# Kernel optimization log

Measured on AMD Instinct MI355X. Metric: run time of the kernel, lower is better.

The kernel has to match this reference:

```python
import jax, jax.numpy as jnp
import numpy as np

B, S, D, Q, N, H = 2, 2048, 4096, 32, 8, 128
ROPE_THETA = 10000.0


def apply_rope(x, positions, head_dim, theta):
    # x: [B, S, heads, H], positions: [B, S] int
    half = head_dim // 2
    inv_freq = 1.0 / (theta ** (jnp.arange(half, dtype=jnp.float32) * 2.0 / head_dim))
    angles = positions.astype(jnp.float32)[..., None] * inv_freq  # [B, S, half]
    cos = jnp.cos(angles)[:, :, None, :]  # [B, S, 1, half]
    sin = jnp.sin(angles)[:, :, None, :]
    x1, x2 = x[..., :half], x[..., half:]
    return jnp.concatenate([x1 * cos - x2 * sin, x2 * cos + x1 * sin], axis=-1).astype(x.dtype)


def setup_inputs() -> dict:
    key = jax.random.key(0)
    ks = jax.random.split(key, 5)
    x = jax.random.normal(ks[0], (B, S, D), dtype=jnp.float32)
    positions = jnp.broadcast_to(jnp.arange(S, dtype=jnp.int32)[None, :], (B, S))
    scale = 0.02
    Wq = jax.random.normal(ks[1], (Q, D, H), dtype=jnp.float32) * scale
    Wk = jax.random.normal(ks[2], (N, D, H), dtype=jnp.float32) * scale
    Wv = jax.random.normal(ks[3], (N, D, H), dtype=jnp.float32) * scale
    Wo = jax.random.normal(ks[4], (Q, H, D), dtype=jnp.float32) * scale
    return {"x": x, "positions": positions, "Wq": Wq, "Wk": Wk, "Wv": Wv, "Wo": Wo}


def reference(x, positions, Wq, Wk, Wv, Wo):
    # Prefill path: QKV proj + RoPE + GQA causal attention + O proj.
    head_repeats = Q // N
    q_BSQH = jnp.einsum('BSD,QDH->BSQH', x, Wq)
    q_BSQH = apply_rope(q_BSQH, positions, H, ROPE_THETA)
    k_BSNH = jnp.einsum('BSD,NDH->BSNH', x, Wk)
    k_BSNH = apply_rope(k_BSNH, positions, H, ROPE_THETA)
    v_BSNH = jnp.einsum('BSD,NDH->BSNH', x, Wv)
    # GQA head repeat
    k_BTQH = jnp.repeat(k_BSNH, head_repeats, axis=2) if head_repeats > 1 else k_BSNH
    v_BTQH = jnp.repeat(v_BSNH, head_repeats, axis=2) if head_repeats > 1 else v_BSNH
    scores_BQST = jnp.einsum('BSQH,BTQH->BQST', q_BSQH, k_BTQH) / jnp.sqrt(jnp.float32(H))
    causal = jnp.tril(jnp.ones((1, 1, S, S), dtype=jnp.bool_))
    scores_BQST = jnp.where(causal, scores_BQST, -jnp.inf)
    weights_BQST = jax.nn.softmax(scores_BQST, axis=-1)
    out_BSQH = jnp.einsum('BQST,BTQH->BSQH', weights_BQST, v_BTQH)
    o_BSD = jnp.einsum('BSQH,QHD->BSD', out_BSQH, Wo)
    return o_BSD
```

## Files before the change

### kernel.cpp

```cpp
#include <hip/hip_runtime.h>
#include <cstdint>
#include <cstddef>

#define B_  2
#define S_  2048
#define D_  4096
#define QH_ 32
#define NH_ 8
#define HD_ 128
#define MROWS (B_ * S_)
#define NQKV  (QH_ * HD_ + 2 * NH_ * HD_)
#define KOFF  (QH_ * HD_)
#define VOFF  (QH_ * HD_ + NH_ * HD_)

typedef __attribute__((ext_vector_type(8))) short bf16x8;
typedef __attribute__((ext_vector_type(4))) float f32x4;

__device__ __forceinline__ unsigned short f2bf(float f) {
    unsigned int u = __float_as_uint(f);
    return (unsigned short)((u + 0x7FFFu + ((u >> 16) & 1u)) >> 16);
}
__device__ __forceinline__ float bf2f(unsigned short h) { return __uint_as_float(((unsigned int)h) << 16); }

__device__ __forceinline__ void gl2lds16(const void* g, void* l) {
    __builtin_amdgcn_global_load_lds(
        (const __attribute__((address_space(1))) void*)g,
        (__attribute__((address_space(3))) void*)l, 16, 0, 0);
}

__global__ __launch_bounds__(256)
void convert_bf16_kernel(const float* __restrict__ in, unsigned short* __restrict__ out)
{
    const size_t i = ((size_t)blockIdx.x * 256 + threadIdx.x) * 8;
    float4 a = *(const float4*)(in + i);
    float4 b = *(const float4*)(in + i + 4);
    uint4 o;
    o.x = (unsigned int)f2bf(a.x) | ((unsigned int)f2bf(a.y) << 16);
    o.y = (unsigned int)f2bf(a.z) | ((unsigned int)f2bf(a.w) << 16);
    o.z = (unsigned int)f2bf(b.x) | ((unsigned int)f2bf(b.y) << 16);
    o.w = (unsigned int)f2bf(b.z) | ((unsigned int)f2bf(b.w) << 16);
    *(uint4*)(out + i) = o;
}

__global__ __launch_bounds__(256)
void transpose_conv_kernel(const float* __restrict__ in, unsigned short* __restrict__ out,
                           int R, int C)
{
    __shared__ unsigned short tile[64][72];
    const int t  = threadIdx.x;
    const int c0 = blockIdx.x * 64;
    const int r0 = blockIdx.y * 64;
    in  += (size_t)blockIdx.z * R * C;
    out += (size_t)blockIdx.z * R * C;
    {
        const int rr = t >> 4;
        const int cc = (t & 15) * 4;
        #pragma unroll
        for (int p = 0; p < 4; ++p) {
            float4 v = *(const float4*)(in + (size_t)(r0 + p * 16 + rr) * C + c0 + cc);
            unsigned int lo = (unsigned int)f2bf(v.x) | ((unsigned int)f2bf(v.y) << 16);
            unsigned int hi = (unsigned int)f2bf(v.z) | ((unsigned int)f2bf(v.w) << 16);
            *(uint2*)&tile[p * 16 + rr][cc] = make_uint2(lo, hi);
        }
    }
    __syncthreads();
    {
        const int j  = t >> 3;
        const int i8 = (t & 7) * 8;
        #pragma unroll
        for (int p = 0; p < 2; ++p) {
            unsigned short tmp[8];
            #pragma unroll
            for (int e = 0; e < 8; ++e) tmp[e] = tile[i8 + e][p * 32 + j];
            *(uint4*)(out + (size_t)(c0 + p * 32 + j) * R + r0 + i8) = *(uint4*)tmp;
        }
    }
}

__global__ __launch_bounds__(256)
void transpose_v_kernel(const unsigned short* __restrict__ qkv, unsigned short* __restrict__ vt)
{
    __shared__ unsigned short tile[64][76];
    const int t  = threadIdx.x;
    const int z  = blockIdx.z;
    const int b  = z >> 3, kh = z & 7;
    const int h0 = blockIdx.x * 64;
    const int s0 = blockIdx.y * 64;
    const unsigned short* in = qkv + (size_t)(b * S_) * NQKV + VOFF + kh * HD_;
    unsigned short* outb = vt + (size_t)z * HD_ * S_;
    {
        const int rr = t >> 4;
        const int cc = (t & 15) * 4;
        #pragma unroll
        for (int p = 0; p < 4; ++p) {
            uint2 v = *(const uint2*)(in + (size_t)(s0 + p * 16 + rr) * NQKV + h0 + cc);
            *(uint2*)&tile[p * 16 + rr][cc] = v;
        }
    }
    __syncthreads();
    {
        const int j  = t >> 3;
        const int i8 = (t & 7) * 8;
        #pragma unroll
        for (int p = 0; p < 2; ++p) {
            unsigned short tmp[8];
            #pragma unroll
            for (int e = 0; e < 8; ++e) tmp[e] = tile[i8 + e][p * 32 + j];
            *(uint4*)(outb + (size_t)(h0 + p * 32 + j) * S_ + s0 + i8) = *(uint4*)tmp;
        }
    }
}

template<int CF32>
__global__ __launch_bounds__(512, 2)
void gemm256_kernel(const unsigned short* __restrict__ A,
                    const unsigned short* __restrict__ Bt,
                    void* __restrict__ Cp, int Nst, int K)
{
    __shared__ alignas(16) unsigned short lds[3][2][256][32];

    const int t = threadIdx.x, l = t & 63, w = t >> 6;
    const int gx  = gridDim.x;
    const int nwg = gx * gridDim.y;
    int lin = blockIdx.y * gx + blockIdx.x;
    lin = (lin & 7) * (nwg >> 3) + (lin >> 3);
    const int bn = (lin % gx) * 256, bm = (lin / gx) * 256;
    const int wr = w >> 2, wc = w & 3;
    const int lm = l & 15, lg = l >> 4;

    f32x4 acc[8][4];
    #pragma unroll
    for (int i = 0; i < 8; ++i)
        #pragma unroll
        for (int j = 0; j < 4; ++j) acc[i][j] = (f32x4){0.f, 0.f, 0.f, 0.f};

    const int srow = w * 16 + (l >> 2);
    const int scol = (((l & 3) - ((l >> 3) & 3)) & 3) * 8;
    const unsigned short* Asrc = A  + (size_t)(bm + srow) * K + scol;
    const unsigned short* Bsrc = Bt + (size_t)(bn + srow) * K + scol;

    const int rcol = ((lg + ((lm >> 1) & 3)) & 3) * 8;

    #define STAGE_A(tt, bb) do {                                                  \
        gl2lds16(Asrc + (size_t)(tt) * 32,                  &lds[bb][0][w*16][0]); \
        gl2lds16(Asrc + (size_t)128*K + (size_t)(tt) * 32,  &lds[bb][0][128 + w*16][0]); } while (0)
    #define STAGE_B(tt, bb) do {                                                  \
        gl2lds16(Bsrc + (size_t)(tt) * 32,                  &lds[bb][1][w*16][0]); \
        gl2lds16(Bsrc + (size_t)128*K + (size_t)(tt) * 32,  &lds[bb][1][128 + w*16][0]); } while (0)

    const int nkt = K >> 5;
    STAGE_A(0, 0); STAGE_B(0, 0);
    STAGE_A(1, 1); STAGE_B(1, 1);

    for (int kt = 0; kt < nkt; ++kt) {
        if (kt + 1 < nkt) asm volatile("s_waitcnt vmcnt(4)" ::: "memory");
        else              asm volatile("s_waitcnt vmcnt(0)" ::: "memory");
        asm volatile("s_barrier" ::: "memory");

        const unsigned short (*bufA)[32] = lds[kt % 3][0];
        const unsigned short (*bufB)[32] = lds[kt % 3][1];
        const int nb = (kt + 2) % 3;
        const bool pf = (kt + 2 < nkt);

        bf16x8 bfr[4], afr[4];
        #pragma unroll
        for (int j = 0; j < 4; ++j) bfr[j] = *(const bf16x8*)&bufB[wc * 64 + j * 16 + lm][rcol];
        #pragma unroll
        for (int i = 0; i < 4; ++i) afr[i] = *(const bf16x8*)&bufA[wr * 128 + i * 16 + lm][rcol];
        if (pf) STAGE_A(kt + 2, nb);
        #pragma unroll
        for (int i = 0; i < 4; ++i)
            #pragma unroll
            for (int j = 0; j < 4; ++j)
                acc[i][j] = __builtin_amdgcn_mfma_f32_16x16x32_bf16(afr[i], bfr[j], acc[i][j], 0, 0, 0);

        #pragma unroll
        for (int i = 0; i < 4; ++i) afr[i] = *(const bf16x8*)&bufA[wr * 128 + (i + 4) * 16 + lm][rcol];
        if (pf) STAGE_B(kt + 2, nb);
        #pragma unroll
        for (int i = 0; i < 4; ++i)
            #pragma unroll
            for (int j = 0; j < 4; ++j)
                acc[i + 4][j] = __builtin_amdgcn_mfma_f32_16x16x32_bf16(afr[i], bfr[j], acc[i + 4][j], 0, 0, 0);
    }
    #undef STAGE_A
    #undef STAGE_B

    const int lr4 = lg * 4;
    #pragma unroll
    for (int i = 0; i < 8; ++i) {
        #pragma unroll
        for (int j = 0; j < 4; ++j) {
            int row = bm + wr * 128 + i * 16 + lr4;
            int col = bn + wc * 64 + j * 16 + lm;
            #pragma unroll
            for (int jj = 0; jj < 4; ++jj) {
                if constexpr (CF32)
                    ((float*)Cp)[(size_t)(row + jj) * Nst + col] = acc[i][j][jj];
                else
                    ((unsigned short*)Cp)[(size_t)(row + jj) * Nst + col] = f2bf(acc[i][j][jj]);
            }
        }
    }
}

template<int LOG2H>
__global__ __launch_bounds__(256)
void rope_kernel(unsigned short* __restrict__ data, const int* __restrict__ positions)
{
    const int gid  = blockIdx.x * 256 + threadIdx.x;
    const int j    = gid & 63;
    const int hr   = gid >> 6;
    const int head = hr & ((1 << LOG2H) - 1);
    const int bs   = hr >> LOG2H;
    const float pos = (float)positions[bs];
    const float inv = expf(-0.14391156831f * (float)j);
    float s, c;
    sincosf(pos * inv, &s, &c);
    const size_t base = (size_t)bs * NQKV + head * HD_;
    const float x1 = bf2f(data[base + j]);
    const float x2 = bf2f(data[base + 64 + j]);
    data[base + j]      = f2bf(x1 * c - x2 * s);
    data[base + 64 + j] = f2bf(x2 * c + x1 * s);
}

__global__ __launch_bounds__(256)
void attn_kernel(const unsigned short* __restrict__ qkv,
                 const unsigned short* __restrict__ vt,
                 unsigned short* __restrict__ ao)
{
    __shared__ alignas(16) unsigned short k_s[2][64][128];
    __shared__ alignas(16) unsigned short v_t[2][128][64];
    __shared__ alignas(16) unsigned short p_s[4][16][72];

    const int t   = threadIdx.x;
    const int blk = blockIdx.x;
    const int sb  = 31 - (blk >> 6);
    const int pr  = blk & 63;
    const int qh  = pr >> 1;
    const int b   = pr & 1;
    const int kh  = qh >> 2;
    const int l   = t & 63, w = t >> 6;
    const int lm  = l & 15;
    const int lg  = l >> 4;
    const int lg4 = lg * 4;
    const int lko = lg * 8;
    const int wrow = w * 16 + lm;
    const int rot  = (lm & 7) * 8;

    const unsigned short* vtb = vt + (size_t)(b * NH_ + kh) * HD_ * S_;
    const size_t kvrow0 = (size_t)(b * S_) * NQKV + KOFF + kh * HD_;

    int ck[4], cv[2];
    #pragma unroll
    for (int kk = 0; kk < 4; ++kk) ck[kk] = (kk * 32 + lko - rot) & 127;
    #pragma unroll
    for (int kk = 0; kk < 2; ++kk) cv[kk] = (kk * 32 + lko - rot) & 63;

    const int krsub = l >> 4, ksseg = (l & 15) * 8;
    const int vrsub = l >> 3, vsseg = (l & 7) * 8;
    #define STAGEKV(cc, bb) do {                                                   \
        const int c64_ = (cc) * 64;                                                \
        _Pragma("unroll")                                                          \
        for (int i_ = 0; i_ < 4; ++i_) {                                           \
            const int kr_ = w * 16 + i_ * 4 + krsub;                               \
            const int ko_ = (ksseg + ((kr_ & 7) << 3)) & 127;                      \
            gl2lds16(qkv + kvrow0 + (size_t)(c64_ + kr_) * NQKV + ko_,             \
                     &k_s[bb][w * 16 + i_ * 4][0]);                                \
        }                                                                          \
        _Pragma("unroll")                                                          \
        for (int i_ = 0; i_ < 4; ++i_) {                                           \
            const int hv_ = w * 32 + i_ * 8 + vrsub;                               \
            const int vo_ = (vsseg + ((hv_ & 7) << 3)) & 63;                       \
            gl2lds16(vtb + (size_t)hv_ * S_ + c64_ + vo_,                          \
                     &v_t[bb][w * 32 + i_ * 8][0]);                                \
        }                                                                          \
    } while (0)

    bf16x8 qf[4];
    {
        const size_t qrow = (size_t)(b * S_ + sb * 64 + wrow) * NQKV + qh * HD_;
        #pragma unroll
        for (int kk = 0; kk < 4; ++kk)
            qf[kk] = *(const bf16x8*)(qkv + qrow + kk * 32 + lko);
    }

    f32x4 acc_o[8];
    #pragma unroll
    for (int i = 0; i < 8; ++i) acc_o[i] = (f32x4){0.f, 0.f, 0.f, 0.f};
    float mreg = -1e30f, lreg = 0.f;

    const float sm_scale = 0.08838834764831845f;

    STAGEKV(0, 0);

    for (int c = 0; c <= sb; ++c) {
        const int cur = c & 1;
        __syncthreads();
        if (c < sb) STAGEKV(c + 1, cur ^ 1);

        f32x4 acc_s[4];
        #pragma unroll
        for (int t4 = 0; t4 < 4; ++t4) acc_s[t4] = (f32x4){0.f, 0.f, 0.f, 0.f};
        #pragma unroll
        for (int kk = 0; kk < 4; ++kk) {
            const bf16x8 qv = qf[kk];
            bf16x8 kf0 = *(const bf16x8*)&k_s[cur][0 * 16 + lm][ck[kk]];
            bf16x8 kf1 = *(const bf16x8*)&k_s[cur][1 * 16 + lm][ck[kk]];
            bf16x8 kf2 = *(const bf16x8*)&k_s[cur][2 * 16 + lm][ck[kk]];
            bf16x8 kf3 = *(const bf16x8*)&k_s[cur][3 * 16 + lm][ck[kk]];
            __builtin_amdgcn_s_setprio(1);
            acc_s[0] = __builtin_amdgcn_mfma_f32_16x16x32_bf16(kf0, qv, acc_s[0], 0, 0, 0);
            acc_s[1] = __builtin_amdgcn_mfma_f32_16x16x32_bf16(kf1, qv, acc_s[1], 0, 0, 0);
            acc_s[2] = __builtin_amdgcn_mfma_f32_16x16x32_bf16(kf2, qv, acc_s[2], 0, 0, 0);
            acc_s[3] = __builtin_amdgcn_mfma_f32_16x16x32_bf16(kf3, qv, acc_s[3], 0, 0, 0);
            __builtin_amdgcn_s_setprio(0);
        }

        const bool diag = (c == sb);
        float p[4][4];
        #pragma unroll
        for (int t4 = 0; t4 < 4; ++t4)
            #pragma unroll
            for (int r = 0; r < 4; ++r) {
                float s = acc_s[t4][r] * sm_scale;
                if (diag && (t4 * 16 + lg4 + r > wrow)) s = -1e30f;
                p[t4][r] = s;
            }
        float mc = p[0][0];
        #pragma unroll
        for (int t4 = 0; t4 < 4; ++t4)
            #pragma unroll
            for (int r = 0; r < 4; ++r) mc = fmaxf(mc, p[t4][r]);
        mc = fmaxf(mc, __shfl_xor(mc, 16, 64));
        mc = fmaxf(mc, __shfl_xor(mc, 32, 64));
        float sf = 1.0f;
        if (mc > mreg + 8.0f) {
            sf = __expf(mreg - mc);
            mreg = mc;
            lreg *= sf;
        }
        if (__any(sf != 1.0f)) {
            #pragma unroll
            for (int r = 0; r < 4; ++r) {
                const float s_r = __shfl(sf, (l & 48) | (lg4 + r), 64);
                #pragma unroll
                for (int ht = 0; ht < 8; ++ht) acc_o[ht][r] *= s_r;
            }
        }
        float ps = 0.f;
        #pragma unroll
        for (int t4 = 0; t4 < 4; ++t4)
            #pragma unroll
            for (int r = 0; r < 4; ++r) {
                p[t4][r] = __expf(p[t4][r] - mreg);
                ps += p[t4][r];
            }
        ps += __shfl_xor(ps, 16, 64);
        ps += __shfl_xor(ps, 32, 64);
        lreg += ps;
        #pragma unroll
        for (int t4 = 0; t4 < 4; ++t4) {
            unsigned int d0 = (unsigned int)f2bf(p[t4][0]) | ((unsigned int)f2bf(p[t4][1]) << 16);
            unsigned int d1 = (unsigned int)f2bf(p[t4][2]) | ((unsigned int)f2bf(p[t4][3]) << 16);
            *(unsigned int*)&p_s[w][lm][t4 * 16 + lg4]     = d0;
            *(unsigned int*)&p_s[w][lm][t4 * 16 + lg4 + 2] = d1;
        }

        #pragma unroll
        for (int kk = 0; kk < 2; ++kk) {
            const bf16x8 pa = *(const bf16x8*)&p_s[w][lm][kk * 32 + lko];
            #pragma unroll
            for (int ht = 0; ht < 8; ht += 4) {
                bf16x8 bv0 = *(const bf16x8*)&v_t[cur][(ht + 0) * 16 + lm][cv[kk]];
                bf16x8 bv1 = *(const bf16x8*)&v_t[cur][(ht + 1) * 16 + lm][cv[kk]];
                bf16x8 bv2 = *(const bf16x8*)&v_t[cur][(ht + 2) * 16 + lm][cv[kk]];
                bf16x8 bv3 = *(const bf16x8*)&v_t[cur][(ht + 3) * 16 + lm][cv[kk]];
                __builtin_amdgcn_s_setprio(1);
                acc_o[ht + 0] = __builtin_amdgcn_mfma_f32_16x16x32_bf16(pa, bv0, acc_o[ht + 0], 0, 0, 0);
                acc_o[ht + 1] = __builtin_amdgcn_mfma_f32_16x16x32_bf16(pa, bv1, acc_o[ht + 1], 0, 0, 0);
                acc_o[ht + 2] = __builtin_amdgcn_mfma_f32_16x16x32_bf16(pa, bv2, acc_o[ht + 2], 0, 0, 0);
                acc_o[ht + 3] = __builtin_amdgcn_mfma_f32_16x16x32_bf16(pa, bv3, acc_o[ht + 3], 0, 0, 0);
                __builtin_amdgcn_s_setprio(0);
            }
        }
    }
    #undef STAGEKV

    #pragma unroll
    for (int r = 0; r < 4; ++r) {
        const float lr = __shfl(lreg, (l & 48) | (lg4 + r), 64);
        const float invl = 1.f / lr;
        const size_t row = (size_t)(b * S_ + sb * 64 + w * 16 + lg4 + r);
        #pragma unroll
        for (int ht = 0; ht < 8; ++ht)
            ao[(row * QH_ + qh) * HD_ + ht * 16 + lm] = f2bf(acc_o[ht][r] * invl);
    }
}

extern "C" void kernel_launch(void* const* d_in, const int* in_sizes, int n_in,
                              void* d_out, int out_size, void* d_ws, size_t ws_size,
                              hipStream_t stream)
{
    const float* x  = (const float*)d_in[0];
    const int*  pos = (const int*)d_in[1];
    const float* Wq = (const float*)d_in[2];
    const float* Wk = (const float*)d_in[3];
    const float* Wv = (const float*)d_in[4];
    const float* Wo = (const float*)d_in[5];
    float* out = (float*)d_out;

    char* wsb = (char*)d_ws;
    unsigned short* qkv = (unsigned short*)(wsb);
    unsigned short* wt  = (unsigned short*)(wsb + 50331648);
    unsigned short* vt  = (unsigned short*)(wsb + 83886080);
    unsigned short* r0  = (unsigned short*)(wsb + 100663296);

    const dim3 blk(256);
    const dim3 blk512(512);
    convert_bf16_kernel<<<8192, blk, 0, stream>>>(x, r0);
    transpose_conv_kernel<<<dim3(2, 64, 32), blk, 0, stream>>>(Wq, wt, D_, HD_);
    transpose_conv_kernel<<<dim3(2, 64, 8),  blk, 0, stream>>>(Wk, wt + (size_t)KOFF * D_, D_, HD_);
    transpose_conv_kernel<<<dim3(2, 64, 8),  blk, 0, stream>>>(Wv, wt + (size_t)VOFF * D_, D_, HD_);
    gemm256_kernel<0><<<dim3(NQKV / 256, MROWS / 256), blk512, 0, stream>>>(r0, wt, qkv, NQKV, D_);
    transpose_conv_kernel<<<dim3(64, 64, 1), blk, 0, stream>>>(Wo, wt, D_, D_);
    transpose_v_kernel<<<dim3(2, 32, 16), blk, 0, stream>>>(qkv, vt);
    rope_kernel<5><<<(MROWS * QH_ * 64) / 256, blk, 0, stream>>>(qkv, pos);
    rope_kernel<3><<<(MROWS * NH_ * 64) / 256, blk, 0, stream>>>(qkv + KOFF, pos);
    attn_kernel<<<B_ * QH_ * (S_ / 64), blk, 0, stream>>>(qkv, vt, r0);
    gemm256_kernel<1><<<dim3(D_ / 256, MROWS / 256), blk512, 0, stream>>>(r0, wt, out, D_, QH_ * HD_);
}
```

Before: 574.0 us.

## Fuse RoPE into QKV GEMM epilogue by remapping B-tile columns

Removes the two standalone RoPE kernels and applies the rotation in the QKV GEMM epilogue. The wave-to-column mapping of the B fragments changes so each lane holds both halves (col and col+64) of a head dimension pair, letting it rotate them in registers before storing. This saves a read-modify-write pass over Q and K plus two launches. In exchange the epilogue does a sincos per row and stores with a 64-column stride instead of the previous layout, which may reduce store coalescing.

```diff
diff --git a/kernel.cpp b/kernel.cpp
--- a/kernel.cpp
+++ b/kernel.cpp
@@ -111,11 +111,12 @@
     }
 }
 
-template<int CF32>
+template<int CF32, int ROPE>
 __global__ __launch_bounds__(512, 2)
 void gemm256_kernel(const unsigned short* __restrict__ A,
                     const unsigned short* __restrict__ Bt,
-                    void* __restrict__ Cp, int Nst, int K)
+                    void* __restrict__ Cp, const int* __restrict__ positions,
+                    int Nst, int K)
 {
     __shared__ alignas(16) unsigned short lds[3][2][256][32];
 
@@ -164,7 +165,7 @@
 
         bf16x8 bfr[4], afr[4];
         #pragma unroll
-        for (int j = 0; j < 4; ++j) bfr[j] = *(const bf16x8*)&bufB[wc * 64 + j * 16 + lm][rcol];
+        for (int j = 0; j < 4; ++j) bfr[j] = *(const bf16x8*)&bufB[j * 64 + wc * 16 + lm][rcol];
         #pragma unroll
         for (int i = 0; i < 4; ++i) afr[i] = *(const bf16x8*)&bufA[wr * 128 + i * 16 + lm][rcol];
         if (pf) STAGE_A(kt + 2, nb);
@@ -187,41 +188,43 @@
     #undef STAGE_B
 
     const int lr4 = lg * 4;
+    float invf = 0.f;
+    if constexpr (ROPE) {
+        const int fi = wc * 16 + lm;
+        invf = expf(-0.14391156831f * (float)fi);
+    }
     #pragma unroll
     for (int i = 0; i < 8; ++i) {
         #pragma unroll
-        for (int j = 0; j < 4; ++j) {
-            int row = bm + wr * 128 + i * 16 + lr4;
-            int col = bn + wc * 64 + j * 16 + lm;
-            #pragma unroll
-            for (int jj = 0; jj < 4; ++jj) {
-                if constexpr (CF32)
-                    ((float*)Cp)[(size_t)(row + jj) * Nst + col] = acc[i][j][jj];
-                else
-                    ((unsigned short*)Cp)[(size_t)(row + jj) * Nst + col] = f2bf(acc[i][j][jj]);
-            }
-        }
-    }
-}
-
-template<int LOG2H>
-__global__ __launch_bounds__(256)
-void rope_kernel(unsigned short* __restrict__ data, const int* __restrict__ positions)
-{
-    const int gid  = blockIdx.x * 256 + threadIdx.x;
-    const int j    = gid & 63;
-    const int hr   = gid >> 6;
-    const int head = hr & ((1 << LOG2H) - 1);
-    const int bs   = hr >> LOG2H;
-    const float pos = (float)positions[bs];
-    const float inv = expf(-0.14391156831f * (float)j);
-    float s, c;
-    sincosf(pos * inv, &s, &c);
-    const size_t base = (size_t)bs * NQKV + head * HD_;
-    const float x1 = bf2f(data[base + j]);
-    const float x2 = bf2f(data[base + 64 + j]);
-    data[base + j]      = f2bf(x1 * c - x2 * s);
-    data[base + 64 + j] = f2bf(x2 * c + x1 * s);
+        for (int jj = 0; jj < 4; ++jj) {
+            const int row = bm + wr * 128 + i * 16 + lr4 + jj;
+            float sn = 0.f, cs = 1.f;
+            if constexpr (ROPE) {
+                const float pos = (float)positions[row];
+                sincosf(pos * invf, &sn, &cs);
+            }
+            #pragma unroll
+            for (int j = 0; j < 4; j += 2) {
+                float x1 = acc[i][j][jj];
+                float x2 = acc[i][j + 1][jj];
+                const int col = bn + j * 64 + wc * 16 + lm;
+                if constexpr (ROPE) {
+                    if (col < VOFF) {
+                        const float o1 = x1 * cs - x2 * sn;
+                        const float o2 = x2 * cs + x1 * sn;
+                        x1 = o1; x2 = o2;
+                    }
+                }
+                if constexpr (CF32) {
+                    ((float*)Cp)[(size_t)row * Nst + col]      = x1;
+                    ((float*)Cp)[(size_t)row * Nst + col + 64] = x2;
+                } else {
+                    ((unsigned short*)Cp)[(size_t)row * Nst + col]      = f2bf(x1);
+                    ((unsigned short*)Cp)[(size_t)row * Nst + col + 64] = f2bf(x2);
+                }
+            }
+        }
+    }
 }
 
 __global__ __launch_bounds__(256)
@@ -422,11 +425,11 @@
     transpose_conv_kernel<<<dim3(2, 64, 32), blk, 0, stream>>>(Wq, wt, D_, HD_);
     transpose_conv_kernel<<<dim3(2, 64, 8),  blk, 0, stream>>>(Wk, wt + (size_t)KOFF * D_, D_, HD_);
     transpose_conv_kernel<<<dim3(2, 64, 8),  blk, 0, stream>>>(Wv, wt + (size_t)VOFF * D_, D_, HD_);
-    gemm256_kernel<0><<<dim3(NQKV / 256, MROWS / 256), blk512, 0, stream>>>(r0, wt, qkv, NQKV, D_);
+    gemm256_kernel<0, 1><<<dim3(NQKV / 256, MROWS / 256), blk512, 0, stream>>>(
+        r0, wt, qkv, pos, NQKV, D_);
     transpose_conv_kernel<<<dim3(64, 64, 1), blk, 0, stream>>>(Wo, wt, D_, D_);
     transpose_v_kernel<<<dim3(2, 32, 16), blk, 0, stream>>>(qkv, vt);
-    rope_kernel<5><<<(MROWS * QH_ * 64) / 256, blk, 0, stream>>>(qkv, pos);
-    rope_kernel<3><<<(MROWS * NH_ * 64) / 256, blk, 0, stream>>>(qkv + KOFF, pos);
     attn_kernel<<<B_ * QH_ * (S_ / 64), blk, 0, stream>>>(qkv, vt, r0);
-    gemm256_kernel<1><<<dim3(D_ / 256, MROWS / 256), blk512, 0, stream>>>(r0, wt, out, D_, QH_ * HD_);
-}
+    gemm256_kernel<1, 0><<<dim3(D_ / 256, MROWS / 256), blk512, 0, stream>>>(
+        r0, wt, out, pos, D_, QH_ * HD_);
+}
```

After: 555.2 us. 3.3% less time.
